# Performance work log

Hardware: AMD Instinct MI355X
Metric: run time of the kernel (lower is better)

Reference implementation:

```python
import jax, jax.numpy as jnp
import numpy as np

VOCAB = 1000
EMB = 64
HID = 64


def _lstm_last(x, mask, Wx, Wh, b):
    """Keras-style LSTM over time, returning final hidden state.

    x:    [T, B, EMB] float
    mask: [T, B] bool  (False = padded step: state carried through, Keras mask_zero semantics)
    Wx:   [EMB, 4H], Wh: [H, 4H], b: [4H]; gate order i, f, g(c), o.
    """
    T, B, _ = x.shape
    h0 = jnp.zeros((B, HID), x.dtype)
    c0 = jnp.zeros((B, HID), x.dtype)

    def step(carry, inp):
        h, c = carry
        x_t, m_t = inp
        z = x_t @ Wx + h @ Wh + b                      # [B, 4H]
        i, f, g, o = jnp.split(z, 4, axis=-1)
        i = jax.nn.sigmoid(i)
        f = jax.nn.sigmoid(f)
        o = jax.nn.sigmoid(o)
        c_new = f * c + i * jnp.tanh(g)
        h_new = o * jnp.tanh(c_new)
        m = m_t[:, None]
        h = jnp.where(m, h_new, h)
        c = jnp.where(m, c_new, c)
        return (h, c), None

    (h_T, _), _ = jax.lax.scan(step, (h0, c0), (x, mask))
    return h_T


def setup_inputs() -> dict:
    key = jax.random.key(0)
    ks = jax.random.split(key, 8)
    B, T = 512, 1024
    tokens = jax.random.randint(ks[0], (B, T), 0, VOCAB, dtype=jnp.int32)
    emb_table = jax.random.normal(ks[1], (VOCAB, EMB), jnp.float32) * 0.05
    def glorot(k, shape):
        lim = np.sqrt(6.0 / (shape[0] + shape[1]))
        return jax.random.uniform(k, shape, jnp.float32, -lim, lim)
    # Keras unit_forget_bias: bias of forget gate initialized to 1.
    b_init = jnp.concatenate([jnp.zeros(HID), jnp.ones(HID), jnp.zeros(2 * HID)]).astype(jnp.float32)
    return {
        "tokens": tokens,
        "emb_table": emb_table,
        "Wx_f": glorot(ks[2], (EMB, 4 * HID)),
        "Wh_f": glorot(ks[3], (HID, 4 * HID)),
        "b_f": b_init,
        "Wx_b": glorot(ks[4], (EMB, 4 * HID)),
        "Wh_b": glorot(ks[5], (HID, 4 * HID)),
        "b_b": b_init,
    }


def reference(tokens, emb_table, Wx_f, Wh_f, b_f, Wx_b, Wh_b, b_b):
    # Embedding with mask_zero=True: token 0 is masked.
    emb = emb_table[tokens]                  # [B, T, EMB]
    mask = tokens != 0                       # [B, T]
    x = jnp.transpose(emb, (1, 0, 2))        # [T, B, EMB]
    m = jnp.transpose(mask, (1, 0))          # [T, B]
    h_fwd = _lstm_last(x, m, Wx_f, Wh_f, b_f)
    # Backward direction: Keras go_backwards reverses the sequence (and mask).
    h_bwd = _lstm_last(x[::-1], m[::-1], Wx_b, Wh_b, b_b)
    return jnp.concatenate([h_fwd, h_bwd], axis=-1)  # [B, 2H]
```

## Files before the change

kernel.cpp:

```cpp
#include <hip/hip_runtime.h>

#define T_STEPS 1024
#define B_TOT   512
#define VOCAB   1000
#define EMB     64
#define HID     64
#define GATES   256

typedef float f4 __attribute__((ext_vector_type(4)));
typedef float f2 __attribute__((ext_vector_type(2)));

__device__ __forceinline__ float fast_rcp(float x)  { return __builtin_amdgcn_rcpf(x); }
__device__ __forceinline__ float fast_exp2(float x) { return __builtin_amdgcn_exp2f(x); }

__device__ __forceinline__ float sigmoid_f(float x) {
    return fast_rcp(1.0f + fast_exp2(-1.4426950408889634f * x));
}
__device__ __forceinline__ float tanh_f(float x) {
    float e = fast_exp2(2.8853900817779268f * x);
    return 1.0f - 2.0f * fast_rcp(e + 1.0f);
}

__device__ __forceinline__ void pk_fma_acc(f2& acc, f2 a, f2 b) {
    asm("v_pk_fma_f32 %0, %1, %2, %0" : "+v"(acc) : "v"(a), "v"(b));
}

__global__ __launch_bounds__(256, 4)
void zx_table_kernel(const float* __restrict__ emb,
                     const float* __restrict__ Wx_f, const float* __restrict__ b_f,
                     const float* __restrict__ Wx_b, const float* __restrict__ b_b,
                     float* __restrict__ zx_tab)
{
    const int bid = blockIdx.x;
    const int dir = bid / VOCAB;
    const int v   = bid - dir * VOCAB;
    const int j   = threadIdx.x;
    const int p   = j & 1;
    const int u   = (j >> 1) & 63;
    const int w   = j >> 7;
    const int col = (2 * w + p) * HID + u;

    const float* __restrict__ Wx = dir ? Wx_b : Wx_f;
    const float* __restrict__ bv = dir ? b_b  : b_f;

    __shared__ float4 x4[EMB / 4];
    if (j < EMB / 4) x4[j] = ((const float4*)emb)[v * (EMB / 4) + j];
    __syncthreads();

    float a0 = bv[col], a1 = 0.f, a2 = 0.f, a3 = 0.f;
#pragma unroll
    for (int q = 0; q < EMB / 4; ++q) {
        float4 xv = x4[q];
        a0 = fmaf(xv.x, Wx[(4 * q + 0) * GATES + col], a0);
        a1 = fmaf(xv.y, Wx[(4 * q + 1) * GATES + col], a1);
        a2 = fmaf(xv.z, Wx[(4 * q + 2) * GATES + col], a2);
        a3 = fmaf(xv.w, Wx[(4 * q + 3) * GATES + col], a3);
    }
    zx_tab[(dir * VOCAB + v) * GATES + j] = (a0 + a1) + (a2 + a3);
}

__global__ __launch_bounds__(128, 2)
void lstm_rec_kernel(const int* __restrict__ tokens,
                     const float* __restrict__ Wh_f,
                     const float* __restrict__ Wh_b,
                     const float* __restrict__ zx_tab,
                     float* __restrict__ out)
{
    const int bx  = blockIdx.x;
    const int dir = bx >> 9;
    const int row = bx & 511;
    const int u   = threadIdx.x & 63;
    const int w   = threadIdx.x >> 6;

    const float* __restrict__ Wh   = dir ? Wh_b : Wh_f;
    const f2*    __restrict__ zx2  = (const f2*)(zx_tab + dir * (VOCAB * GATES));
    const int*   __restrict__ trow = tokens + row * T_STEPS;

    const int colA = (2 * w) * HID + u;
    const int colB = colA + HID;
    f2 whA2[HID / 2], whB2[HID / 2];
#pragma unroll
    for (int m = 0; m < HID / 2; ++m) {
        f2 a; a.x = Wh[(2 * m) * GATES + colA]; a.y = Wh[(2 * m + 1) * GATES + colA];
        whA2[m] = a;
        f2 b; b.x = Wh[(2 * m) * GATES + colB]; b.y = Wh[(2 * m + 1) * GATES + colB];
        whB2[m] = b;
    }

    __shared__ float hbuf[HID];
    __shared__ f2    act2[HID];

    if (threadIdx.x < HID) hbuf[threadIdx.x] = 0.0f;
    float c = 0.0f;
    __syncthreads();

    int tokc = trow[dir ? (T_STEPS - 1) : 0];
    int tokn = trow[dir ? (T_STEPS - 2) : 1];
    f2  zxc  = zx2[tokc * 128 + w * 64 + u];

    const f4* __restrict__ hb4 = (const f4*)hbuf;

#pragma unroll 1
    for (int t = 0; t < T_STEPS; ++t) {
        int t2   = (t + 2 < T_STEPS) ? (t + 2) : (T_STEPS - 1);
        int tokf = trow[dir ? (T_STEPS - 1 - t2) : t2];
        f2  zxn  = zx2[tokn * 128 + w * 64 + u];

        f2 accA0; accA0.x = zxc.x; accA0.y = 0.f;
        f2 accA1; accA1.x = 0.f;   accA1.y = 0.f;
        f2 accB0; accB0.x = zxc.y; accB0.y = 0.f;
        f2 accB1; accB1.x = 0.f;   accB1.y = 0.f;
#pragma unroll
        for (int q = 0; q < HID / 4; ++q) {
            f4 hv = hb4[q];
            f2 hlo; hlo.x = hv.x; hlo.y = hv.y;
            f2 hhi; hhi.x = hv.z; hhi.y = hv.w;
            pk_fma_acc(accA0, hlo, whA2[2 * q]);
            pk_fma_acc(accA1, hhi, whA2[2 * q + 1]);
            pk_fma_acc(accB0, hlo, whB2[2 * q]);
            pk_fma_acc(accB1, hhi, whB2[2 * q + 1]);
        }
        float zA = (accA0.x + accA1.x) + (accA0.y + accA1.y);
        float zB = (accB0.x + accB1.x) + (accB0.y + accB1.y);

        float actA, actB;
        if (w == 0) {
            actA = sigmoid_f(zA);
            actB = sigmoid_f(zB);
        } else {
            actA = tanh_f(zA);
            actB = sigmoid_f(zB);
            f2 go; go.x = actA; go.y = actB;
            act2[u] = go;
        }
        __syncthreads();

        if (w == 0 && tokc != 0) {
            f2 go = act2[u];
            c = fmaf(actB, c, actA * go.x);
            hbuf[u] = go.y * tanh_f(c);
        }
        __syncthreads();

        tokc = tokn; tokn = tokf; zxc = zxn;
    }

    if (w == 0)
        out[row * (2 * HID) + dir * HID + u] = hbuf[u];
}

extern "C" void kernel_launch(void* const* d_in, const int* in_sizes, int n_in,
                              void* d_out, int out_size, void* d_ws, size_t ws_size,
                              hipStream_t stream) {
    const int*   tokens = (const int*)  d_in[0];
    const float* emb    = (const float*)d_in[1];
    const float* Wx_f   = (const float*)d_in[2];
    const float* Wh_f   = (const float*)d_in[3];
    const float* b_f    = (const float*)d_in[4];
    const float* Wx_b   = (const float*)d_in[5];
    const float* Wh_b   = (const float*)d_in[6];
    const float* b_b    = (const float*)d_in[7];
    float* out = (float*)d_out;

    float* zx_tab = (float*)d_ws;

    hipLaunchKernelGGL(zx_table_kernel, dim3(2 * VOCAB), dim3(GATES), 0, stream,
                       emb, Wx_f, b_f, Wx_b, b_b, zx_tab);
    hipLaunchKernelGGL(lstm_rec_kernel, dim3(2 * B_TOT), dim3(128), 0, stream,
                       tokens, Wh_f, Wh_b, zx_tab, out);
}
```

Measured before the change: 596.0 us.

## Compute cell update redundantly in both waves to drop a per-step barrier

Both waves now exchange their gate activations through a parity double-buffered shared array. Each wave then computes the cell and hidden update itself and keeps a private copy of h in its own shared buffer. This removes the second __syncthreads per timestep, which mattered in the latency-bound recurrence loop. The cost is duplicated cell-state and tanh work in the second wave and slightly more shared memory. The final output is taken from a register instead of shared memory.

```diff
diff --git a/kernel.cpp b/kernel.cpp
--- a/kernel.cpp
+++ b/kernel.cpp
@@ -87,18 +87,20 @@
         whB2[m] = b;
     }
 
-    __shared__ float hbuf[HID];
-    __shared__ f2    act2[HID];
+    __shared__ float hb[2][HID];
+    __shared__ f2    acx[2][2][HID];
 
-    if (threadIdx.x < HID) hbuf[threadIdx.x] = 0.0f;
-    float c = 0.0f;
+    if (threadIdx.x < HID) hb[0][threadIdx.x] = 0.0f;
+    else                   hb[1][threadIdx.x - HID] = 0.0f;
+    float c = 0.0f, hval = 0.0f;
+    int   par = 0;
     __syncthreads();
 
     int tokc = trow[dir ? (T_STEPS - 1) : 0];
     int tokn = trow[dir ? (T_STEPS - 2) : 1];
     f2  zxc  = zx2[tokc * 128 + w * 64 + u];
 
-    const f4* __restrict__ hb4 = (const f4*)hbuf;
+    const f4* __restrict__ hb4 = (const f4*)&hb[w][0];
 
 #pragma unroll 1
     for (int t = 0; t < T_STEPS; ++t) {
@@ -123,30 +125,29 @@
         float zA = (accA0.x + accA1.x) + (accA0.y + accA1.y);
         float zB = (accB0.x + accB1.x) + (accB0.y + accB1.y);
 
-        float actA, actB;
-        if (w == 0) {
-            actA = sigmoid_f(zA);
-            actB = sigmoid_f(zB);
-        } else {
-            actA = tanh_f(zA);
-            actB = sigmoid_f(zB);
-            f2 go; go.x = actA; go.y = actB;
-            act2[u] = go;
-        }
+        float actA = (w == 0) ? sigmoid_f(zA) : tanh_f(zA);
+        float actB = sigmoid_f(zB);
+        f2 mine; mine.x = actA; mine.y = actB;
+        acx[par][w][u] = mine;
         __syncthreads();
 
-        if (w == 0 && tokc != 0) {
-            f2 go = act2[u];
-            c = fmaf(actB, c, actA * go.x);
-            hbuf[u] = go.y * tanh_f(c);
+        f2 other = acx[par][w ^ 1][u];
+        float ig = (w == 0) ? actA    : other.x;
+        float fg = (w == 0) ? actB    : other.y;
+        float gg = (w == 0) ? other.x : actA;
+        float og = (w == 0) ? other.y : actB;
+        if (tokc != 0) {
+            c    = fmaf(fg, c, ig * gg);
+            hval = og * tanh_f(c);
+            hb[w][u] = hval;
         }
-        __syncthreads();
+        par ^= 1;
 
         tokc = tokn; tokn = tokf; zxc = zxn;
     }
 
     if (w == 0)
-        out[row * (2 * HID) + dir * HID + u] = hbuf[u];
+        out[row * (2 * HID) + dir * HID + u] = hval;
 }
 
 extern "C" void kernel_launch(void* const* d_in, const int* in_sizes, int n_in,
```

Measured after the change: 657.9 us. +10.4%, slower.
